# Performance work log

Measured on AMD Instinct MI355X. Metric: run time of the kernel, lower is better.

Reference implementation:

```python
import jax, jax.numpy as jnp
import numpy as np

NEG_SLOPE = 0.2  # PyG GATConv default leaky_relu slope


def _gat_layer(x, src, dst, W, a_src, a_dst, b, N, concat):
    # x: [N, F_in]; W: [F_in, H*C]; a_src/a_dst: [H, C]; b: [H*C] or [C]
    H, C = a_src.shape
    h = (x @ W).reshape(N, H, C)                      # [N, H, C]
    al_s = jnp.einsum('nhc,hc->nh', h, a_src)          # [N, H]
    al_d = jnp.einsum('nhc,hc->nh', h, a_dst)          # [N, H]
    e = jax.nn.leaky_relu(al_s[src] + al_d[dst], NEG_SLOPE)  # [E, H]
    # segment softmax over incoming edges of each dst node
    m = jax.ops.segment_max(e, dst, num_segments=N)    # [N, H]
    ex = jnp.exp(e - m[dst])                           # [E, H]
    denom = jax.ops.segment_sum(ex, dst, num_segments=N)
    attn = ex / denom[dst]                             # [E, H]
    msg = (h[src] * attn[:, :, None]).reshape(-1, H * C)  # [E, H*C]
    out = jax.ops.segment_sum(msg, dst, num_segments=N)   # [N, H*C]
    if concat:
        return out + b
    return out.reshape(N, H, C).mean(axis=1) + b


def setup_inputs() -> dict:
    key = jax.random.key(0)
    ks = jax.random.split(key, 20)
    N, E, D, C, H = 20000, 160000, 768, 128, 4
    HC = H * C  # 512
    def glorot(k, shape):
        fan = shape[0] + shape[-1]
        return jax.random.uniform(k, shape, jnp.float32, -1.0, 1.0) * np.sqrt(6.0 / fan)
    inp = {
        'x': jax.random.normal(ks[0], (N, D), jnp.float32),
        'edge_index': jax.random.randint(ks[1], (2, E), 0, N, jnp.int64),
        'W1': glorot(ks[2], (D, HC)),  'as1': glorot(ks[3], (H, C)), 'ad1': glorot(ks[4], (H, C)), 'b1': jnp.zeros((HC,), jnp.float32),
        'W2': glorot(ks[5], (HC, HC)), 'as2': glorot(ks[6], (H, C)), 'ad2': glorot(ks[7], (H, C)), 'b2': jnp.zeros((HC,), jnp.float32),
        'W3': glorot(ks[8], (HC, C)),  'as3': glorot(ks[9], (1, C)), 'ad3': glorot(ks[10], (1, C)), 'b3': jnp.zeros((C,), jnp.float32),
        'Ws1': glorot(ks[11], (C, C // 2)), 'bs1': jnp.zeros((C // 2,), jnp.float32),
        'Ws2': glorot(ks[12], (C // 2, 1)), 'bs2': jnp.zeros((1,), jnp.float32),
    }
    return inp


def reference(x, edge_index, W1, as1, ad1, b1, W2, as2, ad2, b2, W3, as3, ad3, b3, Ws1, bs1, Ws2, bs2):
    N = x.shape[0]
    loops = jnp.arange(N, dtype=edge_index.dtype)
    src = jnp.concatenate([edge_index[0], loops])  # add self-loops (PyG default)
    dst = jnp.concatenate([edge_index[1], loops])
    h = _gat_layer(x, src, dst, W1, as1, ad1, b1, N, concat=True)
    h = jax.nn.relu(h)  # dropout is identity in eval mode
    h = _gat_layer(h, src, dst, W2, as2, ad2, b2, N, concat=True)
    h = jax.nn.relu(h)
    h = _gat_layer(h, src, dst, W3, as3, ad3, b3, N, concat=False)
    # risk scoring head: Linear -> ReLU -> Linear -> Sigmoid
    s = jax.nn.relu(h @ Ws1 + bs1)
    return jax.nn.sigmoid(s @ Ws2 + bs2)  # [N, 1]
```

## Files before the change

kernel.cpp:

```cpp
#include <hip/hip_runtime.h>
#include <hip/hip_bf16.h>
#include <math.h>

#define NEG_SLOPE 0.2f
#define MAXDEG 64

typedef __attribute__((ext_vector_type(8))) __bf16 bf16x8;
typedef __attribute__((ext_vector_type(4))) float f32x4;

__device__ inline float lrelu(float v) { return v > 0.f ? v : NEG_SLOPE * v; }

__device__ inline unsigned short f2bf(float f) {
    __hip_bfloat16 h = __float2bfloat16(f);
    return *reinterpret_cast<unsigned short*>(&h);
}
__device__ inline float bf_lo(unsigned u) { return __uint_as_float(u << 16); }
__device__ inline float bf_hi(unsigned u) { return __uint_as_float(u & 0xffff0000u); }

__device__ inline void gld16(const unsigned short* gp, unsigned short* lp) {
    __builtin_amdgcn_global_load_lds(
        (const __attribute__((address_space(1))) void*)gp,
        (__attribute__((address_space(3))) void*)lp, 16, 0, 0);
}

__device__ inline void transpose_one(const float* __restrict__ in,
                                     unsigned short* __restrict__ out,
                                     int K, int N, int idx) {
    if (idx >= K * N) return;
    int n = idx / K, k = idx % K;
    out[(size_t)n * K + k] = f2bf(in[(size_t)k * N + n]);
}

#define BARRIER()    asm volatile("s_barrier" ::: "memory")
#define WAIT_LGKM0() asm volatile("s_waitcnt lgkmcnt(0)" ::: "memory")
#define WAIT_VM0()   asm volatile("s_waitcnt vmcnt(0)" ::: "memory")
#define WAIT_VM3()   asm volatile("s_waitcnt vmcnt(3)" ::: "memory")
#define WAIT_VM6()   asm volatile("s_waitcnt vmcnt(6)" ::: "memory")

__global__ __launch_bounds__(256) void preproc_kernel(
    const float* __restrict__ x, unsigned short* __restrict__ xbf, int n4,
    const float* __restrict__ W1, unsigned short* __restrict__ W1t,
    const float* __restrict__ W2, unsigned short* __restrict__ W2t,
    const float* __restrict__ W3, unsigned short* __restrict__ W3t,
    const float* __restrict__ Ws1, unsigned short* __restrict__ Ws1t,
    const int* __restrict__ ei, int E, int N,
    int* __restrict__ cursor, int* __restrict__ csr,
    int c0, int c1, int c2, int c3, int c4,
    int D, int HC, int C) {
    int b = blockIdx.x;
    int t = threadIdx.x;
    if (b < c0) {
        int i = b * 256 + t;
        if (i < n4) {
            float4 v = reinterpret_cast<const float4*>(x)[i];
            ushort4 o;
            o.x = f2bf(v.x); o.y = f2bf(v.y); o.z = f2bf(v.z); o.w = f2bf(v.w);
            reinterpret_cast<ushort4*>(xbf)[i] = o;
        }
        return;
    }
    b -= c0;
    if (b < c1) { transpose_one(W1, W1t, D, HC, b * 256 + t); return; }
    b -= c1;
    if (b < c2) { transpose_one(W2, W2t, HC, HC, b * 256 + t); return; }
    b -= c2;
    if (b < c3) { transpose_one(W3, W3t, HC, C, b * 256 + t); return; }
    b -= c3;
    if (b < c4) { transpose_one(Ws1, Ws1t, 128, 64, b * 256 + t); return; }
    b -= c4;
    {
        int e = b * 256 + t;
        if (e < E + N) {
            int src, dst;
            if (e < E) { src = ei[e]; dst = ei[E + e]; }
            else       { src = dst = e - E; }
            int pos = atomicAdd(&cursor[dst], 1);
            if (pos < MAXDEG) csr[dst * MAXDEG + pos] = src;
        }
    }
}

template <int HEADS>
__global__ __launch_bounds__(512) void gemm_big(const unsigned short* __restrict__ A,
                                                const unsigned short* __restrict__ Bt,
                                                unsigned short* __restrict__ Cc,
                                                int M, int N, int K, int rowTiles,
                                                const float* __restrict__ a_src,
                                                const float* __restrict__ a_dst,
                                                float* __restrict__ alS,
                                                float* __restrict__ alD) {
    __shared__ unsigned short Asl[3][128 * 32];
    __shared__ unsigned short Bsl[3][256 * 32];
    const int tid  = threadIdx.x;
    const int lane = tid & 63;
    const int wave = tid >> 6;

    int r, c;
    {
        int b = blockIdx.x;
        int mainRows = rowTiles & ~7;
        int mainBlocks = mainRows * 2;
        if (b < mainBlocks) {
            int xcd = b & 7;
            c = (b >> 3) & 1;
            r = (b >> 4) * 8 + xcd;
        } else {
            int idx = b - mainBlocks;
            r = mainRows + (idx >> 1);
            c = idx & 1;
        }
    }
    const int rowBase = r * 128;
    const int colBase = c * 256;
    const int wm = (wave & 1) * 64;
    const int wn = (wave >> 1) * 64;
    const int q   = lane >> 4;
    const int l16 = lane & 15;

    const int ar  = tid >> 2;
    const int acg = (tid & 3) ^ ((ar >> 1) & 3);
    int gaA = rowBase + ar; if (gaA >= M) gaA = M - 1;
    const unsigned short* gpA0 = A + (size_t)gaA * K + acg * 8;

    const int br0  = tid >> 2;
    const int bcg0 = (tid & 3) ^ ((br0 >> 1) & 3);
    const int br1  = (tid + 512) >> 2;
    const int bcg1 = (tid & 3) ^ ((br1 >> 1) & 3);
    const unsigned short* gpB0 = Bt + (size_t)(colBase + br0) * K + bcg0 * 8;
    const unsigned short* gpB1 = Bt + (size_t)(colBase + br1) * K + bcg1 * 8;

    const int nk = K >> 5;
    f32x4 acc[4][4] = {};

    auto stage = [&](int kt, int buf) {
        gld16(gpA0 + kt * 32, &Asl[buf][tid * 8]);
        gld16(gpB0 + kt * 32, &Bsl[buf][tid * 8]);
        gld16(gpB1 + kt * 32, &Bsl[buf][(size_t)(tid + 512) * 8]);
    };
    auto compute = [&](int buf) {
        bf16x8 af[4], bfv[4];
#pragma unroll
        for (int mi = 0; mi < 4; mi++) {
            int row = wm + mi * 16 + l16;
            int ch = q ^ ((row >> 1) & 3);
            af[mi] = *reinterpret_cast<const bf16x8*>(&Asl[buf][row * 32 + ch * 8]);
        }
#pragma unroll
        for (int ni = 0; ni < 4; ni++) {
            int row = wn + ni * 16 + l16;
            int ch = q ^ ((row >> 1) & 3);
            bfv[ni] = *reinterpret_cast<const bf16x8*>(&Bsl[buf][row * 32 + ch * 8]);
        }
#pragma unroll
        for (int mi = 0; mi < 4; mi++)
#pragma unroll
            for (int ni = 0; ni < 4; ni++)
                acc[mi][ni] = __builtin_amdgcn_mfma_f32_16x16x32_bf16(af[mi], bfv[ni], acc[mi][ni], 0, 0, 0);
    };

    stage(0, 0);
    stage(1, 1);
    int buf = 0;
    for (int kt = 0; kt < nk; kt++) {
        if (kt + 2 < nk) {
            int nbuf = buf + 2; if (nbuf >= 3) nbuf -= 3;
            stage(kt + 2, nbuf);
            WAIT_VM6();
        } else if (kt + 1 < nk) {
            WAIT_VM3();
        } else {
            WAIT_VM0();
        }
        BARRIER();
        compute(buf);
        WAIT_LGKM0();
        BARRIER();
        buf++; if (buf >= 3) buf = 0;
    }

    const int headBase = colBase >> 7;
    const int hl   = wn >> 7;
    const int half = (wn >> 6) & 1;
    const float* aslp = a_src + (headBase + hl) * 128;
    const float* adlp = a_dst + (headBase + hl) * 128;
    float acoef[4], dcoef[4];
#pragma unroll
    for (int ni = 0; ni < 4; ni++) {
        int cl = half * 64 + ni * 16 + l16;
        acoef[ni] = aslp[cl];
        dcoef[ni] = adlp[cl];
    }

    float2* red = reinterpret_cast<float2*>(&Asl[0][0]);

#pragma unroll
    for (int mi = 0; mi < 4; mi++) {
#pragma unroll
        for (int rr = 0; rr < 4; rr++) {
            int lrow = wm + mi * 16 + q * 4 + rr;
            int grow = rowBase + lrow;
            bool ok = grow < M;
            float vs = 0.f, vd = 0.f;
#pragma unroll
            for (int ni = 0; ni < 4; ni++) {
                float hv = acc[mi][ni][rr];
                vs += hv * acoef[ni];
                vd += hv * dcoef[ni];
                if (ok) {
                    int gcol = colBase + wn + ni * 16 + l16;
                    Cc[(size_t)grow * N + gcol] = f2bf(hv);
                }
            }
#pragma unroll
            for (int d = 1; d < 16; d <<= 1) {
                vs += __shfl_xor(vs, d);
                vd += __shfl_xor(vd, d);
            }
            if (l16 == 0) red[lrow * 4 + hl * 2 + half] = make_float2(vs, vd);
        }
    }
    __syncthreads();
    if (tid < 256) {
        int row = tid >> 1, hh = tid & 1;
        int grow = rowBase + row;
        if (grow < M) {
            float2 a = red[row * 4 + hh * 2 + 0];
            float2 b = red[row * 4 + hh * 2 + 1];
            alS[(size_t)grow * HEADS + headBase + hh] = a.x + b.x;
            alD[(size_t)grow * HEADS + headBase + hh] = a.y + b.y;
        }
    }
}

__global__ __launch_bounds__(256) void gemm_l3(const unsigned short* __restrict__ A,
                                               const unsigned short* __restrict__ Bt,
                                               unsigned short* __restrict__ Cc,
                                               int M, int K,
                                               const float* __restrict__ a_src,
                                               const float* __restrict__ a_dst,
                                               float* __restrict__ alS,
                                               float* __restrict__ alD) {
    const int N = 128;
    __shared__ unsigned short Asl[3][64 * 32];
    __shared__ unsigned short Bsl[3][128 * 32];
    const int tid  = threadIdx.x;
    const int lane = tid & 63;
    const int wave = tid >> 6;
    const int rowBase = blockIdx.x * 64;
    const int wm = (wave & 1) * 32;
    const int wn = (wave >> 1) * 64;
    const int q   = lane >> 4;
    const int l16 = lane & 15;

    const int ar  = tid >> 2;
    const int acg = (tid & 3) ^ ((ar >> 1) & 3);
    int gaA = rowBase + ar; if (gaA >= M) gaA = M - 1;
    const unsigned short* gpA0 = A + (size_t)gaA * K + acg * 8;

    const int br0  = tid >> 2;
    const int bcg0 = (tid & 3) ^ ((br0 >> 1) & 3);
    const int br1  = (tid + 256) >> 2;
    const int bcg1 = (tid & 3) ^ ((br1 >> 1) & 3);
    const unsigned short* gpB0 = Bt + (size_t)br0 * K + bcg0 * 8;
    const unsigned short* gpB1 = Bt + (size_t)br1 * K + bcg1 * 8;

    const int nk = K >> 5;
    f32x4 acc[2][4] = {};

    auto stage = [&](int kt, int buf) {
        gld16(gpA0 + kt * 32, &Asl[buf][tid * 8]);
        gld16(gpB0 + kt * 32, &Bsl[buf][tid * 8]);
        gld16(gpB1 + kt * 32, &Bsl[buf][(size_t)(tid + 256) * 8]);
    };
    auto compute = [&](int buf) {
        bf16x8 af[2], bfv[4];
#pragma unroll
        for (int mi = 0; mi < 2; mi++) {
            int row = wm + mi * 16 + l16;
            int ch = q ^ ((row >> 1) & 3);
            af[mi] = *reinterpret_cast<const bf16x8*>(&Asl[buf][row * 32 + ch * 8]);
        }
#pragma unroll
        for (int ni = 0; ni < 4; ni++) {
            int row = wn + ni * 16 + l16;
            int ch = q ^ ((row >> 1) & 3);
            bfv[ni] = *reinterpret_cast<const bf16x8*>(&Bsl[buf][row * 32 + ch * 8]);
        }
#pragma unroll
        for (int mi = 0; mi < 2; mi++)
#pragma unroll
            for (int ni = 0; ni < 4; ni++)
                acc[mi][ni] = __builtin_amdgcn_mfma_f32_16x16x32_bf16(af[mi], bfv[ni], acc[mi][ni], 0, 0, 0);
    };

    stage(0, 0);
    stage(1, 1);
    int buf = 0;
    for (int kt = 0; kt < nk; kt++) {
        if (kt + 2 < nk) {
            int nbuf = buf + 2; if (nbuf >= 3) nbuf -= 3;
            stage(kt + 2, nbuf);
            WAIT_VM6();
        } else if (kt + 1 < nk) {
            WAIT_VM3();
        } else {
            WAIT_VM0();
        }
        BARRIER();
        compute(buf);
        WAIT_LGKM0();
        BARRIER();
        buf++; if (buf >= 3) buf = 0;
    }

    const int half = wn >> 6;
    float acoef[4], dcoef[4];
#pragma unroll
    for (int ni = 0; ni < 4; ni++) {
        int cl = wn + ni * 16 + l16;
        acoef[ni] = a_src[cl];
        dcoef[ni] = a_dst[cl];
    }

    float2* red = reinterpret_cast<float2*>(&Asl[0][0]);

#pragma unroll
    for (int mi = 0; mi < 2; mi++) {
#pragma unroll
        for (int rr = 0; rr < 4; rr++) {
            int lrow = wm + mi * 16 + q * 4 + rr;
            int grow = rowBase + lrow;
            bool ok = grow < M;
            float vs = 0.f, vd = 0.f;
#pragma unroll
            for (int ni = 0; ni < 4; ni++) {
                float hv = acc[mi][ni][rr];
                vs += hv * acoef[ni];
                vd += hv * dcoef[ni];
                if (ok) {
                    int gcol = wn + ni * 16 + l16;
                    Cc[(size_t)grow * N + gcol] = f2bf(hv);
                }
            }
#pragma unroll
            for (int d = 1; d < 16; d <<= 1) {
                vs += __shfl_xor(vs, d);
                vd += __shfl_xor(vd, d);
            }
            if (l16 == 0) red[lrow * 2 + half] = make_float2(vs, vd);
        }
    }
    __syncthreads();
    if (tid < 64) {
        int grow = rowBase + tid;
        if (grow < M) {
            float2 a = red[tid * 2 + 0];
            float2 b = red[tid * 2 + 1];
            alS[grow] = a.x + b.x;
            alD[grow] = a.y + b.y;
        }
    }
}

template <int H, int C, int MODE>
__global__ __launch_bounds__(256) void gat_aggregate(const unsigned short* __restrict__ hb,
                                                     const float* __restrict__ alS,
                                                     const float* __restrict__ alD,
                                                     const int* __restrict__ cursor,
                                                     const int* __restrict__ csr_src,
                                                     const float* __restrict__ bias,
                                                     unsigned short* __restrict__ outbuf,
                                                     int N) {
    constexpr int HC = H * C;
    constexpr int PER = HC / 64;
    __shared__ int   sIdx[4][16];
    __shared__ float sW[4][64];

    int n = (blockIdx.x * blockDim.x + threadIdx.x) >> 6;
    int lane = threadIdx.x & 63;
    int wave = threadIdx.x >> 6;
    if (n >= N) return;
    int total = cursor[n]; if (total > MAXDEG) total = MAXDEG;
    const int* rowp = csr_src + (size_t)n * MAXDEG;

    const int grp  = lane >> 4;
    const int slot = lane & 15;
    const int myh  = (H == 4) ? grp : 0;
    const float adh = alD[n * H + myh];
    const unsigned short* hbl = hb + (size_t)lane * PER;
    const float* sWrow = &sW[wave][grp * 16];

    float m = -1e30f, dn = 0.f;
    float acc0 = 0.f, acc1 = 0.f, acc2 = 0.f, acc3 = 0.f,
          acc4 = 0.f, acc5 = 0.f, acc6 = 0.f, acc7 = 0.f;

    for (int base = 0; base < total; base += 16) {
        int cnt = total - base; if (cnt > 16) cnt = 16;
        bool act = slot < cnt;
        int s_l = rowp[act ? (base + slot) : base];
        float v = act ? lrelu(alS[s_l * H + myh] + adh) : -1e30f;

        float mc = v;
#pragma unroll
        for (int d = 1; d < 16; d <<= 1) mc = fmaxf(mc, __shfl_xor(mc, d));
        float pl = __expf(v - mc);
        float dc = pl;
#pragma unroll
        for (int d = 1; d < 16; d <<= 1) dc += __shfl_xor(dc, d);
        float nm = fmaxf(m, mc);
        float so = __expf(m - nm);
        float sc = __expf(mc - nm);
        dn = dn * so + dc * sc;
        m = nm;
        float wl = pl * sc;

        if (lane < 16) sIdx[wave][lane] = s_l;
        sW[wave][lane] = wl;

        acc0 *= so; acc1 *= so;
        if (PER == 8) {
            acc2 *= so; acc3 *= so; acc4 *= so; acc5 *= so;
            acc6 *= so; acc7 *= so;
        }

        int cntR = (cnt + 3) & ~3;

        if (PER == 8) {
            int4   sI = *reinterpret_cast<const int4*>(&sIdx[wave][0]);
            float4 wv = *reinterpret_cast<const float4*>(&sWrow[0]);
            uint4 gA0 = *reinterpret_cast<const uint4*>(hbl + (size_t)sI.x * HC);
            uint4 gA1 = *reinterpret_cast<const uint4*>(hbl + (size_t)sI.y * HC);
            uint4 gA2 = *reinterpret_cast<const uint4*>(hbl + (size_t)sI.z * HC);
            uint4 gA3 = *reinterpret_cast<const uint4*>(hbl + (size_t)sI.w * HC);
            for (int i = 0; i < cntR; i += 4) {
                int4 sI2 = {}; float4 wv2 = {};
                uint4 gB0 = {}, gB1 = {}, gB2 = {}, gB3 = {};
                if (i + 4 < cntR) {
                    sI2 = *reinterpret_cast<const int4*>(&sIdx[wave][i + 4]);
                    wv2 = *reinterpret_cast<const float4*>(&sWrow[i + 4]);
                    gB0 = *reinterpret_cast<const uint4*>(hbl + (size_t)sI2.x * HC);
                    gB1 = *reinterpret_cast<const uint4*>(hbl + (size_t)sI2.y * HC);
                    gB2 = *reinterpret_cast<const uint4*>(hbl + (size_t)sI2.z * HC);
                    gB3 = *reinterpret_cast<const uint4*>(hbl + (size_t)sI2.w * HC);
                }
#define CONSUME(G, W)                                                   \
                { uint4 rc = G; float w = W;                            \
                  acc0 += bf_lo(rc.x) * w; acc1 += bf_hi(rc.x) * w;     \
                  acc2 += bf_lo(rc.y) * w; acc3 += bf_hi(rc.y) * w;     \
                  acc4 += bf_lo(rc.z) * w; acc5 += bf_hi(rc.z) * w;     \
                  acc6 += bf_lo(rc.w) * w; acc7 += bf_hi(rc.w) * w; }
                CONSUME(gA0, wv.x); CONSUME(gA1, wv.y);
                CONSUME(gA2, wv.z); CONSUME(gA3, wv.w);
#undef CONSUME
                sI = sI2; wv = wv2;
                gA0 = gB0; gA1 = gB1; gA2 = gB2; gA3 = gB3;
            }
        } else {
            int4   sI = *reinterpret_cast<const int4*>(&sIdx[wave][0]);
            float4 wv = *reinterpret_cast<const float4*>(&sWrow[0]);
            unsigned gA0 = *reinterpret_cast<const unsigned*>(hbl + (size_t)sI.x * HC);
            unsigned gA1 = *reinterpret_cast<const unsigned*>(hbl + (size_t)sI.y * HC);
            unsigned gA2 = *reinterpret_cast<const unsigned*>(hbl + (size_t)sI.z * HC);
            unsigned gA3 = *reinterpret_cast<const unsigned*>(hbl + (size_t)sI.w * HC);
            for (int i = 0; i < cntR; i += 4) {
                int4 sI2 = {}; float4 wv2 = {};
                unsigned gB0 = 0, gB1 = 0, gB2 = 0, gB3 = 0;
                if (i + 4 < cntR) {
                    sI2 = *reinterpret_cast<const int4*>(&sIdx[wave][i + 4]);
                    wv2 = *reinterpret_cast<const float4*>(&sWrow[i + 4]);
                    gB0 = *reinterpret_cast<const unsigned*>(hbl + (size_t)sI2.x * HC);
                    gB1 = *reinterpret_cast<const unsigned*>(hbl + (size_t)sI2.y * HC);
                    gB2 = *reinterpret_cast<const unsigned*>(hbl + (size_t)sI2.z * HC);
                    gB3 = *reinterpret_cast<const unsigned*>(hbl + (size_t)sI2.w * HC);
                }
                acc0 += bf_lo(gA0) * wv.x; acc1 += bf_hi(gA0) * wv.x;
                acc0 += bf_lo(gA1) * wv.y; acc1 += bf_hi(gA1) * wv.y;
                acc0 += bf_lo(gA2) * wv.z; acc1 += bf_hi(gA2) * wv.z;
                acc0 += bf_lo(gA3) * wv.w; acc1 += bf_hi(gA3) * wv.w;
                sI = sI2; wv = wv2;
                gA0 = gB0; gA1 = gB1; gA2 = gB2; gA3 = gB3;
            }
        }
    }

    float invd = 1.f / dn;
    unsigned short* op = outbuf + (size_t)n * HC + lane * PER;
    const float* bp = bias + lane * PER;
    if (PER == 8) {
        float o0 = acc0 * invd + bp[0], o1 = acc1 * invd + bp[1];
        float o2 = acc2 * invd + bp[2], o3 = acc3 * invd + bp[3];
        float o4 = acc4 * invd + bp[4], o5 = acc5 * invd + bp[5];
        float o6 = acc6 * invd + bp[6], o7 = acc7 * invd + bp[7];
        if (MODE == 0) {
            o0 = fmaxf(o0, 0.f); o1 = fmaxf(o1, 0.f); o2 = fmaxf(o2, 0.f); o3 = fmaxf(o3, 0.f);
            o4 = fmaxf(o4, 0.f); o5 = fmaxf(o5, 0.f); o6 = fmaxf(o6, 0.f); o7 = fmaxf(o7, 0.f);
        }
        op[0] = f2bf(o0); op[1] = f2bf(o1); op[2] = f2bf(o2); op[3] = f2bf(o3);
        op[4] = f2bf(o4); op[5] = f2bf(o5); op[6] = f2bf(o6); op[7] = f2bf(o7);
    } else {
        float o0 = acc0 * invd + bp[0], o1 = acc1 * invd + bp[1];
        if (MODE == 0) { o0 = fmaxf(o0, 0.f); o1 = fmaxf(o1, 0.f); }
        op[0] = f2bf(o0); op[1] = f2bf(o1);
    }
}

__global__ __launch_bounds__(256) void head_mfma(const unsigned short* __restrict__ H3,
                                                 const unsigned short* __restrict__ W1t,
                                                 const float* __restrict__ bs1,
                                                 const float* __restrict__ Ws2,
                                                 const float* __restrict__ bs2,
                                                 float* __restrict__ out, int M) {
    __shared__ unsigned short Asl[128 * 128];
    __shared__ unsigned short Bsl[64 * 128];
    const int tid = threadIdx.x, lane = tid & 63, wave = tid >> 6;
    const int q = lane >> 4, l16 = lane & 15;
    const int rowBase = blockIdx.x * 128;
    const int r0 = tid >> 4;
    const int cg = (tid & 15) ^ (r0 & 7);

#pragma unroll
    for (int it = 0; it < 8; it++) {
        int s = it * 256 + tid;
        int r = it * 16 + r0;
        int ga = rowBase + r; if (ga >= M) ga = M - 1;
        const unsigned short* gp = H3 + (size_t)ga * 128 + cg * 8;
        gld16(gp, &Asl[(size_t)s * 8]);
    }
#pragma unroll
    for (int it = 0; it < 4; it++) {
        int s = it * 256 + tid;
        int r = it * 16 + r0;
        const unsigned short* gp = W1t + (size_t)r * 128 + cg * 8;
        gld16(gp, &Bsl[(size_t)s * 8]);
    }
    __syncthreads();

    const int wm = wave * 32;
    f32x4 acc[2][4] = {};
#pragma unroll
    for (int kh = 0; kh < 4; kh++) {
        bf16x8 af[2], bfv[4];
#pragma unroll
        for (int mi = 0; mi < 2; mi++) {
            int row = wm + mi * 16 + l16;
            int ch = (kh * 4 + q) ^ (row & 7);
            af[mi] = *reinterpret_cast<const bf16x8*>(&Asl[row * 128 + ch * 8]);
        }
#pragma unroll
        for (int ni = 0; ni < 4; ni++) {
            int row = ni * 16 + l16;
            int ch = (kh * 4 + q) ^ (row & 7);
            bfv[ni] = *reinterpret_cast<const bf16x8*>(&Bsl[row * 128 + ch * 8]);
        }
#pragma unroll
        for (int mi = 0; mi < 2; mi++)
#pragma unroll
            for (int ni = 0; ni < 4; ni++)
                acc[mi][ni] = __builtin_amdgcn_mfma_f32_16x16x32_bf16(af[mi], bfv[ni], acc[mi][ni], 0, 0, 0);
    }
    __syncthreads();

    float b1v[4], w2v[4];
#pragma unroll
    for (int ni = 0; ni < 4; ni++) {
        int cI = ni * 16 + l16;
        b1v[ni] = bs1[cI];
        w2v[ni] = Ws2[cI];
    }
    float* red = reinterpret_cast<float*>(Bsl);
#pragma unroll
    for (int mi = 0; mi < 2; mi++) {
#pragma unroll
        for (int r = 0; r < 4; r++) {
            int lrow = wm + mi * 16 + q * 4 + r;
            float p = 0.f;
#pragma unroll
            for (int ni = 0; ni < 4; ni++)
                p += fmaxf(acc[mi][ni][r] + b1v[ni], 0.f) * w2v[ni];
#pragma unroll
            for (int d = 1; d < 16; d <<= 1) p += __shfl_xor(p, d);
            if (l16 == 0) red[lrow] = p;
        }
    }
    __syncthreads();
    if (tid < 128) {
        int g = rowBase + tid;
        if (g < M) out[g] = 1.f / (1.f + __expf(-(red[tid] + bs2[0])));
    }
}

extern "C" void kernel_launch(void* const* d_in, const int* in_sizes, int n_in,
                              void* d_out, int out_size, void* d_ws, size_t ws_size,
                              hipStream_t stream) {
    const float* x   = (const float*)d_in[0];
    const int*   ei  = (const int*)d_in[1];
    const float* W1  = (const float*)d_in[2];
    const float* as1 = (const float*)d_in[3];
    const float* ad1 = (const float*)d_in[4];
    const float* b1  = (const float*)d_in[5];
    const float* W2  = (const float*)d_in[6];
    const float* as2 = (const float*)d_in[7];
    const float* ad2 = (const float*)d_in[8];
    const float* b2  = (const float*)d_in[9];
    const float* W3  = (const float*)d_in[10];
    const float* as3 = (const float*)d_in[11];
    const float* ad3 = (const float*)d_in[12];
    const float* b3  = (const float*)d_in[13];
    const float* Ws1 = (const float*)d_in[14];
    const float* bs1 = (const float*)d_in[15];
    const float* Ws2 = (const float*)d_in[16];
    const float* bs2 = (const float*)d_in[17];

    const int N = out_size;
    const int E = in_sizes[1] / 2;
    const int D = in_sizes[0] / N;
    const int HC = 512, H = 4, C = 128;
    const int Etot = E + N;

    char* p = (char*)d_ws;
    auto alloc = [&](size_t bytes) -> void* {
        void* q = (void*)p;
        p += (bytes + 255) & ~(size_t)255;
        return q;
    };
    char*  zbeg   = p;
    int*   cursor = (int*)alloc((size_t)N * 4);
    char*  zend   = p;
    float* alS1   = (float*)alloc((size_t)N * H * 4);
    float* alD1   = (float*)alloc((size_t)N * H * 4);
    float* alS2   = (float*)alloc((size_t)N * H * 4);
    float* alD2   = (float*)alloc((size_t)N * H * 4);
    float* alS3   = (float*)alloc((size_t)N * 4);
    float* alD3   = (float*)alloc((size_t)N * 4);
    int*   csr    = (int*)alloc((size_t)N * MAXDEG * 4);
    unsigned short* hbuf = (unsigned short*)alloc((size_t)N * HC * 2);
    unsigned short* h3bf = (unsigned short*)alloc((size_t)N * C * 2);
    unsigned short* obf  = (unsigned short*)alloc((size_t)N * HC * 2);
    unsigned short* xbf  = (unsigned short*)alloc((size_t)N * D * 2);
    unsigned short* W1t  = (unsigned short*)alloc((size_t)D * HC * 2);
    unsigned short* W2t  = (unsigned short*)alloc((size_t)HC * HC * 2);
    unsigned short* W3t  = (unsigned short*)alloc((size_t)HC * C * 2);
    unsigned short* Ws1t = (unsigned short*)alloc((size_t)C * 64 * 2);

    hipMemsetAsync(zbeg, 0, (size_t)(zend - zbeg), stream);

    {
        int n4 = N * D / 4;
        int c0 = (n4 + 255) / 256;
        int c1 = (D * HC + 255) / 256;
        int c2 = (HC * HC + 255) / 256;
        int c3 = (HC * C + 255) / 256;
        int c4 = (128 * 64 + 255) / 256;
        int c5 = (Etot + 255) / 256;
        int total = c0 + c1 + c2 + c3 + c4 + c5;
        preproc_kernel<<<total, 256, 0, stream>>>(
            x, xbf, n4, W1, W1t, W2, W2t, W3, W3t, Ws1, Ws1t,
            ei, E, N, cursor, csr, c0, c1, c2, c3, c4, D, HC, C);
    }

    int node_blocks = (N + 3) / 4;
    int rowTiles128 = (N + 127) / 128;
    int rowTiles64  = (N + 63) / 64;
    int headTiles   = (N + 127) / 128;

    gemm_big<4><<<rowTiles128 * 2, 512, 0, stream>>>(
        xbf, W1t, hbuf, N, HC, D, rowTiles128, as1, ad1, alS1, alD1);
    gat_aggregate<4, 128, 0><<<node_blocks, 256, 0, stream>>>(
        hbuf, alS1, alD1, cursor, csr, b1, obf, N);

    gemm_big<4><<<rowTiles128 * 2, 512, 0, stream>>>(
        obf, W2t, hbuf, N, HC, HC, rowTiles128, as2, ad2, alS2, alD2);
    gat_aggregate<4, 128, 0><<<node_blocks, 256, 0, stream>>>(
        hbuf, alS2, alD2, cursor, csr, b2, obf, N);

    gemm_l3<<<rowTiles64, 256, 0, stream>>>(
        obf, W3t, hbuf, N, HC, as3, ad3, alS3, alD3);
    gat_aggregate<1, 128, 2><<<node_blocks, 256, 0, stream>>>(
        hbuf, alS3, alD3, cursor, csr, b3, h3bf, N);

    head_mfma<<<headTiles, 256, 0, stream>>>(h3bf, Ws1t, bs1, Ws2, bs2, (float*)d_out, N);
}
```

Before: 289.1 us.

## Fuse scoring head into last GAT aggregation and issue all gathers before softmax

```diff
diff --git a/kernel.cpp b/kernel.cpp
--- a/kernel.cpp
+++ b/kernel.cpp
@@ -370,25 +370,31 @@
                                                      const int* __restrict__ csr_src,
                                                      const float* __restrict__ bias,
                                                      unsigned short* __restrict__ outbuf,
-                                                     int N) {
+                                                     int N,
+                                                     const unsigned short* __restrict__ Ws1t,
+                                                     const float* __restrict__ bs1,
+                                                     const float* __restrict__ Ws2,
+                                                     const float* __restrict__ bs2,
+                                                     float* __restrict__ out) {
     constexpr int HC = H * C;
     constexpr int PER = HC / 64;
-    __shared__ int   sIdx[4][16];
-    __shared__ float sW[4][64];
+    __shared__ float hrow[4][128];
 
     int n = (blockIdx.x * blockDim.x + threadIdx.x) >> 6;
     int lane = threadIdx.x & 63;
     int wave = threadIdx.x >> 6;
     if (n >= N) return;
-    int total = cursor[n]; if (total > MAXDEG) total = MAXDEG;
     const int* rowp = csr_src + (size_t)n * MAXDEG;
 
     const int grp  = lane >> 4;
     const int slot = lane & 15;
+    const int gbase = lane & 48;
     const int myh  = (H == 4) ? grp : 0;
+    const unsigned short* hbl = hb + (size_t)lane * PER;
+
+    int total = cursor[n];
     const float adh = alD[n * H + myh];
-    const unsigned short* hbl = hb + (size_t)lane * PER;
-    const float* sWrow = &sW[wave][grp * 16];
+    if (total > MAXDEG) total = MAXDEG;
 
     float m = -1e30f, dn = 0.f;
     float acc0 = 0.f, acc1 = 0.f, acc2 = 0.f, acc3 = 0.f,
@@ -396,10 +402,32 @@
 
     for (int base = 0; base < total; base += 16) {
         int cnt = total - base; if (cnt > 16) cnt = 16;
+        int cntR = (cnt + 3) & ~3;
         bool act = slot < cnt;
-        int s_l = rowp[act ? (base + slot) : base];
-        float v = act ? lrelu(alS[s_l * H + myh] + adh) : -1e30f;
-
+
+        int s_raw = rowp[base + slot];
+        int s_safe = ((unsigned)s_raw < (unsigned)N) ? s_raw : 0;
+        float av = alS[(size_t)s_safe * H + myh];
+
+        uint4 g0 = {}, g1 = {}, g2 = {}, g3 = {};
+        uint4 g4 = {}, g5 = {}, g6 = {}, g7 = {};
+        uint4 g8 = {}, g9 = {}, g10 = {}, g11 = {};
+        uint4 g12 = {}, g13 = {}, g14 = {}, g15 = {};
+        unsigned h0 = 0, h1 = 0, h2 = 0, h3 = 0;
+        unsigned h4 = 0, h5 = 0, h6 = 0, h7 = 0;
+        unsigned h8 = 0, h9 = 0, h10 = 0, h11 = 0;
+        unsigned h12 = 0, h13 = 0, h14 = 0, h15 = 0;
+#define LOADQ(GI, HI, J)                                                       \
+        { int ix = __shfl(s_safe, J);                                          \
+          if (PER == 8) GI = *reinterpret_cast<const uint4*>(hbl + (size_t)ix * HC); \
+          else          HI = *reinterpret_cast<const unsigned*>(hbl + (size_t)ix * HC); }
+        LOADQ(g0, h0, 0) LOADQ(g1, h1, 1) LOADQ(g2, h2, 2) LOADQ(g3, h3, 3)
+        if (cntR > 4)  { LOADQ(g4, h4, 4)   LOADQ(g5, h5, 5)   LOADQ(g6, h6, 6)   LOADQ(g7, h7, 7) }
+        if (cntR > 8)  { LOADQ(g8, h8, 8)   LOADQ(g9, h9, 9)   LOADQ(g10, h10, 10) LOADQ(g11, h11, 11) }
+        if (cntR > 12) { LOADQ(g12, h12, 12) LOADQ(g13, h13, 13) LOADQ(g14, h14, 14) LOADQ(g15, h15, 15) }
+#undef LOADQ
+
+        float v = act ? lrelu(av + adh) : -1e30f;
         float mc = v;
 #pragma unroll
         for (int d = 1; d < 16; d <<= 1) mc = fmaxf(mc, __shfl_xor(mc, d));
@@ -414,178 +442,67 @@
         m = nm;
         float wl = pl * sc;
 
-        if (lane < 16) sIdx[wave][lane] = s_l;
-        sW[wave][lane] = wl;
-
         acc0 *= so; acc1 *= so;
         if (PER == 8) {
             acc2 *= so; acc3 *= so; acc4 *= so; acc5 *= so;
             acc6 *= so; acc7 *= so;
         }
 
-        int cntR = (cnt + 3) & ~3;
-
         if (PER == 8) {
-            int4   sI = *reinterpret_cast<const int4*>(&sIdx[wave][0]);
-            float4 wv = *reinterpret_cast<const float4*>(&sWrow[0]);
-            uint4 gA0 = *reinterpret_cast<const uint4*>(hbl + (size_t)sI.x * HC);
-            uint4 gA1 = *reinterpret_cast<const uint4*>(hbl + (size_t)sI.y * HC);
-            uint4 gA2 = *reinterpret_cast<const uint4*>(hbl + (size_t)sI.z * HC);
-            uint4 gA3 = *reinterpret_cast<const uint4*>(hbl + (size_t)sI.w * HC);
-            for (int i = 0; i < cntR; i += 4) {
-                int4 sI2 = {}; float4 wv2 = {};
-                uint4 gB0 = {}, gB1 = {}, gB2 = {}, gB3 = {};
-                if (i + 4 < cntR) {
-                    sI2 = *reinterpret_cast<const int4*>(&sIdx[wave][i + 4]);
-                    wv2 = *reinterpret_cast<const float4*>(&sWrow[i + 4]);
-                    gB0 = *reinterpret_cast<const uint4*>(hbl + (size_t)sI2.x * HC);
-                    gB1 = *reinterpret_cast<const uint4*>(hbl + (size_t)sI2.y * HC);
-                    gB2 = *reinterpret_cast<const uint4*>(hbl + (size_t)sI2.z * HC);
-                    gB3 = *reinterpret_cast<const uint4*>(hbl + (size_t)sI2.w * HC);
-                }
-#define CONSUME(G, W)                                                   \
-                { uint4 rc = G; float w = W;                            \
-                  acc0 += bf_lo(rc.x) * w; acc1 += bf_hi(rc.x) * w;     \
-                  acc2 += bf_lo(rc.y) * w; acc3 += bf_hi(rc.y) * w;     \
-                  acc4 += bf_lo(rc.z) * w; acc5 += bf_hi(rc.z) * w;     \
-                  acc6 += bf_lo(rc.w) * w; acc7 += bf_hi(rc.w) * w; }
-                CONSUME(gA0, wv.x); CONSUME(gA1, wv.y);
-                CONSUME(gA2, wv.z); CONSUME(gA3, wv.w);
+#define CONSUME(G, J)                                                   \
+            { uint4 rc = G; float w = __shfl(wl, gbase | J);            \
+              acc0 += bf_lo(rc.x) * w; acc1 += bf_hi(rc.x) * w;         \
+              acc2 += bf_lo(rc.y) * w; acc3 += bf_hi(rc.y) * w;         \
+              acc4 += bf_lo(rc.z) * w; acc5 += bf_hi(rc.z) * w;         \
+              acc6 += bf_lo(rc.w) * w; acc7 += bf_hi(rc.w) * w; }
+            CONSUME(g0, 0) CONSUME(g1, 1) CONSUME(g2, 2) CONSUME(g3, 3)
+            if (cntR > 4)  { CONSUME(g4, 4)   CONSUME(g5, 5)   CONSUME(g6, 6)   CONSUME(g7, 7) }
+            if (cntR > 8)  { CONSUME(g8, 8)   CONSUME(g9, 9)   CONSUME(g10, 10) CONSUME(g11, 11) }
+            if (cntR > 12) { CONSUME(g12, 12) CONSUME(g13, 13) CONSUME(g14, 14) CONSUME(g15, 15) }
 #undef CONSUME
-                sI = sI2; wv = wv2;
-                gA0 = gB0; gA1 = gB1; gA2 = gB2; gA3 = gB3;
-            }
         } else {
-            int4   sI = *reinterpret_cast<const int4*>(&sIdx[wave][0]);
-            float4 wv = *reinterpret_cast<const float4*>(&sWrow[0]);
-            unsigned gA0 = *reinterpret_cast<const unsigned*>(hbl + (size_t)sI.x * HC);
-            unsigned gA1 = *reinterpret_cast<const unsigned*>(hbl + (size_t)sI.y * HC);
-            unsigned gA2 = *reinterpret_cast<const unsigned*>(hbl + (size_t)sI.z * HC);
-            unsigned gA3 = *reinterpret_cast<const unsigned*>(hbl + (size_t)sI.w * HC);
-            for (int i = 0; i < cntR; i += 4) {
-                int4 sI2 = {}; float4 wv2 = {};
-                unsigned gB0 = 0, gB1 = 0, gB2 = 0, gB3 = 0;
-                if (i + 4 < cntR) {
-                    sI2 = *reinterpret_cast<const int4*>(&sIdx[wave][i + 4]);
-                    wv2 = *reinterpret_cast<const float4*>(&sWrow[i + 4]);
-                    gB0 = *reinterpret_cast<const unsigned*>(hbl + (size_t)sI2.x * HC);
-                    gB1 = *reinterpret_cast<const unsigned*>(hbl + (size_t)sI2.y * HC);
-                    gB2 = *reinterpret_cast<const unsigned*>(hbl + (size_t)sI2.z * HC);
-                    gB3 = *reinterpret_cast<const unsigned*>(hbl + (size_t)sI2.w * HC);
-                }
-                acc0 += bf_lo(gA0) * wv.x; acc1 += bf_hi(gA0) * wv.x;
-                acc0 += bf_lo(gA1) * wv.y; acc1 += bf_hi(gA1) * wv.y;
-                acc0 += bf_lo(gA2) * wv.z; acc1 += bf_hi(gA2) * wv.z;
-                acc0 += bf_lo(gA3) * wv.w; acc1 += bf_hi(gA3) * wv.w;
-                sI = sI2; wv = wv2;
-                gA0 = gB0; gA1 = gB1; gA2 = gB2; gA3 = gB3;
-            }
+#define CONSUME(HV, J)                                                  \
+            { unsigned rc = HV; float w = __shfl(wl, gbase | J);        \
+              acc0 += bf_lo(rc) * w; acc1 += bf_hi(rc) * w; }
+            CONSUME(h0, 0) CONSUME(h1, 1) CONSUME(h2, 2) CONSUME(h3, 3)
+            if (cntR > 4)  { CONSUME(h4, 4)   CONSUME(h5, 5)   CONSUME(h6, 6)   CONSUME(h7, 7) }
+            if (cntR > 8)  { CONSUME(h8, 8)   CONSUME(h9, 9)   CONSUME(h10, 10) CONSUME(h11, 11) }
+            if (cntR > 12) { CONSUME(h12, 12) CONSUME(h13, 13) CONSUME(h14, 14) CONSUME(h15, 15) }
+#undef CONSUME
         }
     }
 
     float invd = 1.f / dn;
-    unsigned short* op = outbuf + (size_t)n * HC + lane * PER;
     const float* bp = bias + lane * PER;
-    if (PER == 8) {
+    if (MODE == 0) {
+        unsigned short* op = outbuf + (size_t)n * HC + lane * PER;
         float o0 = acc0 * invd + bp[0], o1 = acc1 * invd + bp[1];
         float o2 = acc2 * invd + bp[2], o3 = acc3 * invd + bp[3];
         float o4 = acc4 * invd + bp[4], o5 = acc5 * invd + bp[5];
         float o6 = acc6 * invd + bp[6], o7 = acc7 * invd + bp[7];
-        if (MODE == 0) {
-            o0 = fmaxf(o0, 0.f); o1 = fmaxf(o1, 0.f); o2 = fmaxf(o2, 0.f); o3 = fmaxf(o3, 0.f);
-            o4 = fmaxf(o4, 0.f); o5 = fmaxf(o5, 0.f); o6 = fmaxf(o6, 0.f); o7 = fmaxf(o7, 0.f);
-        }
+        o0 = fmaxf(o0, 0.f); o1 = fmaxf(o1, 0.f); o2 = fmaxf(o2, 0.f); o3 = fmaxf(o3, 0.f);
+        o4 = fmaxf(o4, 0.f); o5 = fmaxf(o5, 0.f); o6 = fmaxf(o6, 0.f); o7 = fmaxf(o7, 0.f);
         op[0] = f2bf(o0); op[1] = f2bf(o1); op[2] = f2bf(o2); op[3] = f2bf(o3);
         op[4] = f2bf(o4); op[5] = f2bf(o5); op[6] = f2bf(o6); op[7] = f2bf(o7);
     } else {
         float o0 = acc0 * invd + bp[0], o1 = acc1 * invd + bp[1];
-        if (MODE == 0) { o0 = fmaxf(o0, 0.f); o1 = fmaxf(o1, 0.f); }
-        op[0] = f2bf(o0); op[1] = f2bf(o1);
-    }
-}
-
-__global__ __launch_bounds__(256) void head_mfma(const unsigned short* __restrict__ H3,
-                                                 const unsigned short* __restrict__ W1t,
-                                                 const float* __restrict__ bs1,
-                                                 const float* __restrict__ Ws2,
-                                                 const float* __restrict__ bs2,
-                                                 float* __restrict__ out, int M) {
-    __shared__ unsigned short Asl[128 * 128];
-    __shared__ unsigned short Bsl[64 * 128];
-    const int tid = threadIdx.x, lane = tid & 63, wave = tid >> 6;
-    const int q = lane >> 4, l16 = lane & 15;
-    const int rowBase = blockIdx.x * 128;
-    const int r0 = tid >> 4;
-    const int cg = (tid & 15) ^ (r0 & 7);
-
-#pragma unroll
-    for (int it = 0; it < 8; it++) {
-        int s = it * 256 + tid;
-        int r = it * 16 + r0;
-        int ga = rowBase + r; if (ga >= M) ga = M - 1;
-        const unsigned short* gp = H3 + (size_t)ga * 128 + cg * 8;
-        gld16(gp, &Asl[(size_t)s * 8]);
-    }
-#pragma unroll
-    for (int it = 0; it < 4; it++) {
-        int s = it * 256 + tid;
-        int r = it * 16 + r0;
-        const unsigned short* gp = W1t + (size_t)r * 128 + cg * 8;
-        gld16(gp, &Bsl[(size_t)s * 8]);
-    }
-    __syncthreads();
-
-    const int wm = wave * 32;
-    f32x4 acc[2][4] = {};
-#pragma unroll
-    for (int kh = 0; kh < 4; kh++) {
-        bf16x8 af[2], bfv[4];
-#pragma unroll
-        for (int mi = 0; mi < 2; mi++) {
-            int row = wm + mi * 16 + l16;
-            int ch = (kh * 4 + q) ^ (row & 7);
-            af[mi] = *reinterpret_cast<const bf16x8*>(&Asl[row * 128 + ch * 8]);
-        }
-#pragma unroll
-        for (int ni = 0; ni < 4; ni++) {
-            int row = ni * 16 + l16;
-            int ch = (kh * 4 + q) ^ (row & 7);
-            bfv[ni] = *reinterpret_cast<const bf16x8*>(&Bsl[row * 128 + ch * 8]);
-        }
-#pragma unroll
-        for (int mi = 0; mi < 2; mi++)
-#pragma unroll
-            for (int ni = 0; ni < 4; ni++)
-                acc[mi][ni] = __builtin_amdgcn_mfma_f32_16x16x32_bf16(af[mi], bfv[ni], acc[mi][ni], 0, 0, 0);
-    }
-    __syncthreads();
-
-    float b1v[4], w2v[4];
-#pragma unroll
-    for (int ni = 0; ni < 4; ni++) {
-        int cI = ni * 16 + l16;
-        b1v[ni] = bs1[cI];
-        w2v[ni] = Ws2[cI];
-    }
-    float* red = reinterpret_cast<float*>(Bsl);
-#pragma unroll
-    for (int mi = 0; mi < 2; mi++) {
-#pragma unroll
-        for (int r = 0; r < 4; r++) {
-            int lrow = wm + mi * 16 + q * 4 + r;
-            float p = 0.f;
-#pragma unroll
-            for (int ni = 0; ni < 4; ni++)
-                p += fmaxf(acc[mi][ni][r] + b1v[ni], 0.f) * w2v[ni];
-#pragma unroll
-            for (int d = 1; d < 16; d <<= 1) p += __shfl_xor(p, d);
-            if (l16 == 0) red[lrow] = p;
-        }
-    }
-    __syncthreads();
-    if (tid < 128) {
-        int g = rowBase + tid;
-        if (g < M) out[g] = 1.f / (1.f + __expf(-(red[tid] + bs2[0])));
+        reinterpret_cast<float2*>(&hrow[wave][0])[lane] = make_float2(o0, o1);
+        WAIT_LGKM0();
+        const float* hr = &hrow[wave][0];
+        const unsigned short* wrow = Ws1t + (size_t)lane * 128;
+        float s = bs1[lane];
+#pragma unroll
+        for (int k = 0; k < 128; k += 8) {
+            uint4 wv = *reinterpret_cast<const uint4*>(&wrow[k]);
+            s += hr[k + 0] * bf_lo(wv.x) + hr[k + 1] * bf_hi(wv.x)
+               + hr[k + 2] * bf_lo(wv.y) + hr[k + 3] * bf_hi(wv.y)
+               + hr[k + 4] * bf_lo(wv.z) + hr[k + 5] * bf_hi(wv.z)
+               + hr[k + 6] * bf_lo(wv.w) + hr[k + 7] * bf_hi(wv.w);
+        }
+        float p = fmaxf(s, 0.f) * Ws2[lane];
+#pragma unroll
+        for (int d = 1; d < 64; d <<= 1) p += __shfl_xor(p, d);
+        if (lane == 0) out[n] = 1.f / (1.f + __expf(-(p + bs2[0])));
     }
 }
 
@@ -634,7 +551,6 @@
     float* alD3   = (float*)alloc((size_t)N * 4);
     int*   csr    = (int*)alloc((size_t)N * MAXDEG * 4);
     unsigned short* hbuf = (unsigned short*)alloc((size_t)N * HC * 2);
-    unsigned short* h3bf = (unsigned short*)alloc((size_t)N * C * 2);
     unsigned short* obf  = (unsigned short*)alloc((size_t)N * HC * 2);
     unsigned short* xbf  = (unsigned short*)alloc((size_t)N * D * 2);
     unsigned short* W1t  = (unsigned short*)alloc((size_t)D * HC * 2);
@@ -661,22 +577,22 @@
     int node_blocks = (N + 3) / 4;
     int rowTiles128 = (N + 127) / 128;
     int rowTiles64  = (N + 63) / 64;
-    int headTiles   = (N + 127) / 128;
 
     gemm_big<4><<<rowTiles128 * 2, 512, 0, stream>>>(
         xbf, W1t, hbuf, N, HC, D, rowTiles128, as1, ad1, alS1, alD1);
     gat_aggregate<4, 128, 0><<<node_blocks, 256, 0, stream>>>(
-        hbuf, alS1, alD1, cursor, csr, b1, obf, N);
+        hbuf, alS1, alD1, cursor, csr, b1, obf, N,
+        nullptr, nullptr, nullptr, nullptr, nullptr);
 
     gemm_big<4><<<rowTiles128 * 2, 512, 0, stream>>>(
         obf, W2t, hbuf, N, HC, HC, rowTiles128, as2, ad2, alS2, alD2);
     gat_aggregate<4, 128, 0><<<node_blocks, 256, 0, stream>>>(
-        hbuf, alS2, alD2, cursor, csr, b2, obf, N);
+        hbuf, alS2, alD2, cursor, csr, b2, obf, N,
+        nullptr, nullptr, nullptr, nullptr, nullptr);
 
     gemm_l3<<<rowTiles64, 256, 0, stream>>>(
         obf, W3t, hbuf, N, HC, as3, ad3, alS3, alD3);
     gat_aggregate<1, 128, 2><<<node_blocks, 256, 0, stream>>>(
-        hbuf, alS3, alD3, cursor, csr, b3, h3bf, N);
-
-    head_mfma<<<headTiles, 256, 0, stream>>>(h3bf, Ws1t, bs1, Ws2, bs2, (float*)d_out, N);
-}
+        hbuf, alS3, alD3, cursor, csr, b3, nullptr, N,
+        Ws1t, bs1, Ws2, bs2, (float*)d_out);
+}
```

New measurement: 314.7 us. 8.8% more time.
